# Kernel tuning notes

Measured on AMD Instinct MI355X. Metric: run time of the kernel, lower is better.

The kernel has to match this reference:

```python
import jax, jax.numpy as jnp
import numpy as np

N_NODES = 100000
N_EDGES = 1600000
EMB = 128
EDGE_DIMS = [6, 3]
BN_EPS = 1e-5


def setup_inputs() -> dict:
    key = jax.random.key(0)
    ks = jax.random.split(key, 16)
    inp = {
        "node_feats": jax.random.normal(ks[0], (N_NODES, EMB), jnp.float32),
        "edge_feat_0": jax.random.uniform(ks[1], (N_EDGES, EDGE_DIMS[0]), jnp.float32),
        "edge_feat_1": jax.random.uniform(ks[2], (N_EDGES, EDGE_DIMS[1]), jnp.float32),
        "src": jax.random.randint(ks[3], (N_EDGES,), 0, N_NODES, jnp.int32),
        "dst": jax.random.randint(ks[4], (N_EDGES,), 0, N_NODES, jnp.int32),
    }
    # edge embedding linears (MLP num_layers==1 -> plain Linear)
    s0 = 1.0 / np.sqrt(EDGE_DIMS[0])
    s1 = 1.0 / np.sqrt(EDGE_DIMS[1])
    inp["We0"] = jax.random.uniform(ks[5], (EDGE_DIMS[0], EMB), jnp.float32, -s0, s0)
    inp["be0"] = jax.random.uniform(ks[6], (EMB,), jnp.float32, -s0, s0)
    inp["We1"] = jax.random.uniform(ks[7], (EDGE_DIMS[1], EMB), jnp.float32, -s1, s1)
    inp["be1"] = jax.random.uniform(ks[8], (EMB,), jnp.float32, -s1, s1)
    # mlp: Linear(emb, 2*emb) -> ReLU -> Linear(2*emb, emb)
    sm = 1.0 / np.sqrt(EMB)
    sh = 1.0 / np.sqrt(2 * EMB)
    inp["W1"] = jax.random.uniform(ks[9], (EMB, 2 * EMB), jnp.float32, -sm, sm)
    inp["b1"] = jax.random.uniform(ks[10], (2 * EMB,), jnp.float32, -sm, sm)
    inp["W2"] = jax.random.uniform(ks[11], (2 * EMB, EMB), jnp.float32, -sh, sh)
    inp["b2"] = jax.random.uniform(ks[12], (EMB,), jnp.float32, -sh, sh)
    # batch norm affine params
    inp["gamma"] = jnp.ones((EMB,), jnp.float32)
    inp["beta"] = jnp.zeros((EMB,), jnp.float32)
    return inp


def reference(node_feats, edge_feat_0, edge_feat_1, src, dst,
              We0, be0, We1, be1, W1, b1, W2, b2, gamma, beta):
    n_nodes = node_feats.shape[0]
    # per-family edge embeddings, summed
    edge_embs = (edge_feat_0 @ We0 + be0) + (edge_feat_1 @ We1 + be1)  # [E, D]
    # u_add_e: gather src node feats, add edge emb
    msgs = node_feats[src] + edge_embs  # [E, D]
    # scatter-sum to destination nodes
    agg = jax.ops.segment_sum(msgs, dst, num_segments=n_nodes)  # [N, D]
    # MLP: Linear -> ReLU -> Linear
    h = jax.nn.relu(agg @ W1 + b1) @ W2 + b2  # [N, D]
    # BatchNorm1d (training mode: batch statistics, biased variance)
    mean = jnp.mean(h, axis=0)
    var = jnp.var(h, axis=0)
    h = (h - mean) * jax.lax.rsqrt(var + BN_EPS) * gamma + beta
    return h
```

## Files before the change

### kernel.cpp

```cpp
#include <hip/hip_runtime.h>

#define N_NODES 100000
#define N_EDGES 1600000
#define EMB 128
#define BM 16
#define NSLAB 64
#define BN_EPS 1e-5f

#define SCAN_BLK 512
#define NB_SCAN ((N_NODES + SCAN_BLK - 1) / SCAN_BLK)
#define NPAD (NB_SCAN * SCAN_BLK)

typedef short short8 __attribute__((ext_vector_type(8)));
typedef float floatx4 __attribute__((ext_vector_type(4)));

__device__ __forceinline__ ushort f2bf(float x) {
    unsigned u = __float_as_uint(x);
    u += 0x7fffu + ((u >> 16) & 1u);
    return (ushort)(u >> 16);
}
__device__ __forceinline__ float lo2f(unsigned p) {
    return __uint_as_float(p << 16);
}
__device__ __forceinline__ float hi2f(unsigned p) {
    return __uint_as_float(p & 0xffff0000u);
}

#define DPP_ADD(x, ctrl, mask) \
    ((x) + __int_as_float(__builtin_amdgcn_update_dpp(0, __float_as_int(x), ctrl, mask, 0xf, true)))

__device__ __forceinline__ float wave_sum63(float x) {
    x = DPP_ADD(x, 0x111, 0xf);
    x = DPP_ADD(x, 0x112, 0xf);
    x = DPP_ADD(x, 0x114, 0xf);
    x = DPP_ADD(x, 0x118, 0xf);
    x = DPP_ADD(x, 0x142, 0xa);
    x = DPP_ADD(x, 0x143, 0xc);
    return __int_as_float(__builtin_amdgcn_readlane(__float_as_int(x), 63));
}

__global__ __launch_bounds__(256) void setup_kernel(
    const float* __restrict__ nf, ushort* __restrict__ nfbf,
    const int* __restrict__ dst, int* __restrict__ counts,
    const float* __restrict__ W1, const float* __restrict__ W2,
    ushort* __restrict__ w1f, ushort* __restrict__ w2f)
{
    int gtid = blockIdx.x * 256 + threadIdx.x;
    long gstride = (long)gridDim.x * 256;

    if (gtid < 65536) {
        int idx = gtid;
        int i = idx & 7;
        int lane = (idx >> 3) & 63;
        int kloc = ((lane >> 4) << 3) + i;
        int nloc = lane & 15;
        if (idx < 32768) {
            int ks = (idx >> 9) & 3, nt = idx >> 11;
            w1f[idx] = f2bf(W1[(ks * 32 + kloc) * 256 + nt * 16 + nloc]);
        } else {
            int j = idx - 32768;
            int ks = (j >> 9) & 7, nt = j >> 12;
            w2f[j] = f2bf(W2[(ks * 32 + kloc) * 128 + nt * 16 + nloc]);
        }
    }

    long total = (long)N_NODES * EMB / 4;
    for (long p = gtid; p < total; p += gstride) {
        float4 v = ((const float4*)nf)[p];
        ushort4 o;
        o.x = f2bf(v.x); o.y = f2bf(v.y); o.z = f2bf(v.z); o.w = f2bf(v.w);
        ((ushort4*)nfbf)[p] = o;
    }

    for (long e = gtid; e < N_EDGES; e += gstride)
        atomicAdd(&counts[dst[e]], 1);
}

__global__ __launch_bounds__(SCAN_BLK) void scan_blocksum_kernel(
    const int* __restrict__ counts, int* __restrict__ blockSums)
{
    __shared__ int red[SCAN_BLK];
    int t = threadIdx.x;
    int i = blockIdx.x * SCAN_BLK + t;
    red[t] = (i < N_NODES) ? counts[i] : 0;
    __syncthreads();
    for (int s = SCAN_BLK / 2; s > 0; s >>= 1) {
        if (t < s) red[t] += red[t + s];
        __syncthreads();
    }
    if (t == 0) blockSums[blockIdx.x] = red[0];
}

__global__ __launch_bounds__(SCAN_BLK) void scan_final_kernel(
    const int* __restrict__ counts, const int* __restrict__ blockSums,
    int* __restrict__ offsets, int* __restrict__ cursor)
{
    __shared__ int s[SCAN_BLK];
    __shared__ int bs[256];
    int t = threadIdx.x;
    if (t < 256) bs[t] = (t < NB_SCAN) ? blockSums[t] : 0;
    __syncthreads();
    for (int off = 1; off < 256; off <<= 1) {
        int v = (t < 256 && t >= off) ? bs[t - off] : 0;
        __syncthreads();
        if (t < 256) bs[t] += v;
        __syncthreads();
    }
    int blockBase = (blockIdx.x == 0) ? 0 : bs[blockIdx.x - 1];

    int i = blockIdx.x * SCAN_BLK + t;
    int orig = (i < N_NODES) ? counts[i] : 0;
    s[t] = orig;
    __syncthreads();
    for (int off = 1; off < SCAN_BLK; off <<= 1) {
        int v = (t >= off) ? s[t - off] : 0;
        __syncthreads();
        s[t] += v;
        __syncthreads();
    }
    int excl = s[t] - orig + blockBase;
    if (i < N_NODES) { offsets[i] = excl; cursor[i] = excl; }
    if (i == N_NODES) offsets[N_NODES] = N_EDGES;
}

__global__ __launch_bounds__(256) void scatter24_kernel(
    const int* __restrict__ src, const int* __restrict__ dst,
    const float* __restrict__ ef0, const float* __restrict__ ef1,
    int* __restrict__ cursor, int* __restrict__ rec24)
{
    int e = blockIdx.x * 256 + threadIdx.x;
    if (e >= N_EDGES) return;
    int t = dst[e];
    int pos = atomicAdd(&cursor[t], 1);

    const float2* p0 = (const float2*)(ef0 + (long)e * 6);
    float2 q0 = p0[0], q1 = p0[1], q2 = p0[2];
    const float* p1 = ef1 + (long)e * 3;
    float g0 = p1[0], g1 = p1[1], g2 = p1[2];

    unsigned u0 = (unsigned)f2bf(q0.x) | ((unsigned)f2bf(q0.y) << 16);
    unsigned u1 = (unsigned)f2bf(q1.x) | ((unsigned)f2bf(q1.y) << 16);
    unsigned u2 = (unsigned)f2bf(q2.x) | ((unsigned)f2bf(q2.y) << 16);
    unsigned u3 = (unsigned)f2bf(g0)   | ((unsigned)f2bf(g1) << 16);
    unsigned u4 = (unsigned)f2bf(g2);

    int2* out = (int2*)(rec24 + (long)pos * 6);
    out[0] = make_int2(src[e], (int)u0);
    out[1] = make_int2((int)u1, (int)u2);
    out[2] = make_int2((int)u3, (int)u4);
}

__device__ __forceinline__ void gather_full_chunks(
    int& base, int end, int lane, int q, int lp,
    const int* __restrict__ rec24, const int4* __restrict__ nf16,
    float4& accA, float4& accB, float* fs)
{
    for (; base + 64 <= end; base += 64) {
        const int2* rp = (const int2*)(rec24 + (long)(base + lane) * 6);
        int2 ra = rp[0], rb = rp[1], rc = rp[2];
        int sid = ra.x;
        fs[0] += lo2f((unsigned)ra.y); fs[1] += hi2f((unsigned)ra.y);
        fs[2] += lo2f((unsigned)rb.x); fs[3] += hi2f((unsigned)rb.x);
        fs[4] += lo2f((unsigned)rb.y); fs[5] += hi2f((unsigned)rb.y);
        fs[6] += lo2f((unsigned)rc.x); fs[7] += hi2f((unsigned)rc.x);
        fs[8] += lo2f((unsigned)rc.y);
#pragma unroll 4
        for (int j = 0; j < 16; ++j) {
            int s = __shfl(sid, 4 * j + q);
            int4 nv = nf16[(long)s * 16 + lp];
            accA.x += lo2f((unsigned)nv.x); accA.y += hi2f((unsigned)nv.x);
            accA.z += lo2f((unsigned)nv.y); accA.w += hi2f((unsigned)nv.y);
            accB.x += lo2f((unsigned)nv.z); accB.y += hi2f((unsigned)nv.z);
            accB.z += lo2f((unsigned)nv.w); accB.w += hi2f((unsigned)nv.w);
        }
    }
}

__global__ __launch_bounds__(256, 8) void gather4_kernel(
    const ushort* __restrict__ nfbf, const int* __restrict__ rec24,
    const int* __restrict__ offsets,
    const float* __restrict__ We0, const float* __restrict__ be0,
    const float* __restrict__ We1, const float* __restrict__ be1,
    float* __restrict__ agg)
{
    int wv = threadIdx.x >> 6, lane = threadIdx.x & 63;
    int n0 = blockIdx.x * 8 + wv * 2;
    int q = lane >> 4, lp = lane & 15;
    const int4* nf16 = (const int4*)nfbf;

    int beg0 = offsets[n0];
    int mid  = offsets[n0 + 1];
    int end1 = offsets[n0 + 2];

    float4 a0A = make_float4(0.f, 0.f, 0.f, 0.f), a0B = a0A;
    float4 a1A = a0A, a1B = a0A;
    float fs0[9] = {}, fs1[9] = {};

    int b0 = beg0, b1 = mid;
    gather_full_chunks(b0, mid, lane, q, lp, rec24, nf16, a0A, a0B, fs0);
    gather_full_chunks(b1, end1, lane, q, lp, rec24, nf16, a1A, a1B, fs1);

    int m0 = mid - b0, m1 = end1 - b1;
    int sid0 = 0, sid1 = 0;
    if (lane < m0) {
        const int2* rp = (const int2*)(rec24 + (long)(b0 + lane) * 6);
        int2 ra = rp[0], rb = rp[1], rc = rp[2];
        sid0 = ra.x;
        fs0[0] += lo2f((unsigned)ra.y); fs0[1] += hi2f((unsigned)ra.y);
        fs0[2] += lo2f((unsigned)rb.x); fs0[3] += hi2f((unsigned)rb.x);
        fs0[4] += lo2f((unsigned)rb.y); fs0[5] += hi2f((unsigned)rb.y);
        fs0[6] += lo2f((unsigned)rc.x); fs0[7] += hi2f((unsigned)rc.x);
        fs0[8] += lo2f((unsigned)rc.y);
    }
    if (lane < m1) {
        const int2* rp = (const int2*)(rec24 + (long)(b1 + lane) * 6);
        int2 ra = rp[0], rb = rp[1], rc = rp[2];
        sid1 = ra.x;
        fs1[0] += lo2f((unsigned)ra.y); fs1[1] += hi2f((unsigned)ra.y);
        fs1[2] += lo2f((unsigned)rb.x); fs1[3] += hi2f((unsigned)rb.x);
        fs1[4] += lo2f((unsigned)rb.y); fs1[5] += hi2f((unsigned)rb.y);
        fs1[6] += lo2f((unsigned)rc.x); fs1[7] += hi2f((unsigned)rc.x);
        fs1[8] += lo2f((unsigned)rc.y);
    }
    int mx = m0 > m1 ? m0 : m1;
    int rounds = (mx + 3) >> 2;
#pragma unroll 4
    for (int j = 0; j < rounds; ++j) {
        int r = 4 * j + q;
        int s0 = __shfl(sid0, r);
        int s1 = __shfl(sid1, r);
        if (r < m0) {
            int4 nv = nf16[(long)s0 * 16 + lp];
            a0A.x += lo2f((unsigned)nv.x); a0A.y += hi2f((unsigned)nv.x);
            a0A.z += lo2f((unsigned)nv.y); a0A.w += hi2f((unsigned)nv.y);
            a0B.x += lo2f((unsigned)nv.z); a0B.y += hi2f((unsigned)nv.z);
            a0B.z += lo2f((unsigned)nv.w); a0B.w += hi2f((unsigned)nv.w);
        }
        if (r < m1) {
            int4 nv = nf16[(long)s1 * 16 + lp];
            a1A.x += lo2f((unsigned)nv.x); a1A.y += hi2f((unsigned)nv.x);
            a1A.z += lo2f((unsigned)nv.y); a1A.w += hi2f((unsigned)nv.y);
            a1B.x += lo2f((unsigned)nv.z); a1B.y += hi2f((unsigned)nv.z);
            a1B.z += lo2f((unsigned)nv.w); a1B.w += hi2f((unsigned)nv.w);
        }
    }

#define QRED(v) v += __shfl_xor(v, 16); v += __shfl_xor(v, 32);
    QRED(a0A.x) QRED(a0A.y) QRED(a0A.z) QRED(a0A.w)
    QRED(a0B.x) QRED(a0B.y) QRED(a0B.z) QRED(a0B.w)
    QRED(a1A.x) QRED(a1A.y) QRED(a1A.z) QRED(a1A.w)
    QRED(a1B.x) QRED(a1B.y) QRED(a1B.z) QRED(a1B.w)
#undef QRED

    float fk0[9], fk1[9];
#pragma unroll
    for (int k = 0; k < 9; ++k) {
        fk0[k] = wave_sum63(fs0[k]);
        fk1[k] = wave_sum63(fs1[k]);
    }

    if (q < 2) {
        bool f0 = (q == 0);
        long myn = f0 ? (long)n0 : (long)(n0 + 1);
        float deg = f0 ? (float)(mid - beg0) : (float)(end1 - mid);
        float4 accA, accB;
        accA.x = f0 ? a0A.x : a1A.x; accA.y = f0 ? a0A.y : a1A.y;
        accA.z = f0 ? a0A.z : a1A.z; accA.w = f0 ? a0A.w : a1A.w;
        accB.x = f0 ? a0B.x : a1B.x; accB.y = f0 ? a0B.y : a1B.y;
        accB.z = f0 ? a0B.z : a1B.z; accB.w = f0 ? a0B.w : a1B.w;
        float fkk[9];
#pragma unroll
        for (int k = 0; k < 9; ++k) fkk[k] = f0 ? fk0[k] : fk1[k];

        float4 bA = ((const float4*)be0)[2 * lp];
        float4 bB = ((const float4*)be0)[2 * lp + 1];
        float4 cA = ((const float4*)be1)[2 * lp];
        float4 cB = ((const float4*)be1)[2 * lp + 1];
        float4 eA, eB;
        eA.x = deg * (bA.x + cA.x); eA.y = deg * (bA.y + cA.y);
        eA.z = deg * (bA.z + cA.z); eA.w = deg * (bA.w + cA.w);
        eB.x = deg * (bB.x + cB.x); eB.y = deg * (bB.y + cB.y);
        eB.z = deg * (bB.z + cB.z); eB.w = deg * (bB.w + cB.w);
#pragma unroll
        for (int k = 0; k < 6; ++k) {
            float4 wA = ((const float4*)We0)[k * 32 + 2 * lp];
            float4 wB = ((const float4*)We0)[k * 32 + 2 * lp + 1];
            eA.x = fmaf(fkk[k], wA.x, eA.x); eA.y = fmaf(fkk[k], wA.y, eA.y);
            eA.z = fmaf(fkk[k], wA.z, eA.z); eA.w = fmaf(fkk[k], wA.w, eA.w);
            eB.x = fmaf(fkk[k], wB.x, eB.x); eB.y = fmaf(fkk[k], wB.y, eB.y);
            eB.z = fmaf(fkk[k], wB.z, eB.z); eB.w = fmaf(fkk[k], wB.w, eB.w);
        }
#pragma unroll
        for (int k = 0; k < 3; ++k) {
            float4 wA = ((const float4*)We1)[k * 32 + 2 * lp];
            float4 wB = ((const float4*)We1)[k * 32 + 2 * lp + 1];
            eA.x = fmaf(fkk[6 + k], wA.x, eA.x); eA.y = fmaf(fkk[6 + k], wA.y, eA.y);
            eA.z = fmaf(fkk[6 + k], wA.z, eA.z); eA.w = fmaf(fkk[6 + k], wA.w, eA.w);
            eB.x = fmaf(fkk[6 + k], wB.x, eB.x); eB.y = fmaf(fkk[6 + k], wB.y, eB.y);
            eB.z = fmaf(fkk[6 + k], wB.z, eB.z); eB.w = fmaf(fkk[6 + k], wB.w, eB.w);
        }
        float4 oA = make_float4(accA.x + eA.x, accA.y + eA.y, accA.z + eA.z, accA.w + eA.w);
        float4 oB = make_float4(accB.x + eB.x, accB.y + eB.y, accB.z + eB.z, accB.w + eB.w);
        ((float4*)agg)[myn * 32 + 2 * lp] = oA;
        ((float4*)agg)[myn * 32 + 2 * lp + 1] = oB;
    }
}

__global__ __launch_bounds__(256) void edge_scatter_kernel(
    const float* __restrict__ node_feats,
    const float* __restrict__ ef0,
    const float* __restrict__ ef1,
    const int* __restrict__ src,
    const int* __restrict__ dst,
    const float* __restrict__ We0, const float* __restrict__ be0,
    const float* __restrict__ We1, const float* __restrict__ be1,
    float* __restrict__ agg)
{
    __shared__ float wS[10 * EMB];
    int tid = threadIdx.x;
    for (int i = tid; i < 6 * EMB; i += 256) wS[i] = We0[i];
    for (int i = tid; i < 3 * EMB; i += 256) wS[6 * EMB + i] = We1[i];
    if (tid < EMB) wS[9 * EMB + tid] = be0[tid] + be1[tid];
    __syncthreads();

    int e = blockIdx.x * 2 + (tid >> 7);
    if (e >= N_EDGES) return;
    int d = tid & 127;
    int s = src[e];
    int t = dst[e];
    const float* f0 = ef0 + (long)e * 6;
    const float* f1 = ef1 + (long)e * 3;

    float emb = wS[9 * EMB + d];
#pragma unroll
    for (int k = 0; k < 6; ++k) emb = fmaf(f0[k], wS[k * EMB + d], emb);
#pragma unroll
    for (int k = 0; k < 3; ++k) emb = fmaf(f1[k], wS[6 * EMB + k * EMB + d], emb);

    float val = node_feats[(long)s * EMB + d] + emb;
    atomicAdd(&agg[(long)t * EMB + d], val);
}

__global__ __launch_bounds__(256) void mlp_mfma_kernel(
    float* __restrict__ h,
    const ushort* __restrict__ w1f, const ushort* __restrict__ w2f,
    const float* __restrict__ b1, const float* __restrict__ b2,
    float* __restrict__ stats)
{
    __shared__ __align__(16) char h1S[32 * 512];

    int tid = threadIdx.x;
    int lane = tid & 63;
    int wv = tid >> 6;
    long base = (long)blockIdx.x * 32;

    float4 araw[2][4][2];
#pragma unroll
    for (int mt = 0; mt < 2; ++mt)
#pragma unroll
        for (int ks = 0; ks < 4; ++ks) {
            long row = base + mt * 16 + (lane & 15);
            const float4* p = (const float4*)(h + row * EMB + ks * 32 + ((lane >> 4) << 3));
            araw[mt][ks][0] = p[0];
            araw[mt][ks][1] = p[1];
        }
    __syncthreads();

    short8 a[2][4];
#pragma unroll
    for (int mt = 0; mt < 2; ++mt)
#pragma unroll
        for (int ks = 0; ks < 4; ++ks) {
            union { ushort u[8]; short8 v; } pk;
            float4 x = araw[mt][ks][0], y = araw[mt][ks][1];
            pk.u[0] = f2bf(x.x); pk.u[1] = f2bf(x.y); pk.u[2] = f2bf(x.z); pk.u[3] = f2bf(x.w);
            pk.u[4] = f2bf(y.x); pk.u[5] = f2bf(y.y); pk.u[6] = f2bf(y.z); pk.u[7] = f2bf(y.w);
            a[mt][ks] = pk.v;
        }

    floatx4 acc1[2][4];
#pragma unroll
    for (int nt = 0; nt < 4; ++nt) {
        float bias = b1[(wv * 4 + nt) * 16 + (lane & 15)];
#pragma unroll
        for (int mt = 0; mt < 2; ++mt)
            acc1[mt][nt] = (floatx4){bias, bias, bias, bias};
    }
#pragma unroll
    for (int ks = 0; ks < 4; ++ks) {
#pragma unroll
        for (int nt = 0; nt < 4; ++nt) {
            short8 b = *(const short8*)&w1f[(((wv * 4 + nt) * 4 + ks) * 64 + lane) * 8];
            acc1[0][nt] = __builtin_amdgcn_mfma_f32_16x16x32_bf16(a[0][ks], b, acc1[0][nt], 0, 0, 0);
            acc1[1][nt] = __builtin_amdgcn_mfma_f32_16x16x32_bf16(a[1][ks], b, acc1[1][nt], 0, 0, 0);
        }
    }
#pragma unroll
    for (int mt = 0; mt < 2; ++mt)
#pragma unroll
        for (int nt = 0; nt < 4; ++nt)
#pragma unroll
            for (int i = 0; i < 4; ++i) {
                int row = mt * 16 + ((lane >> 4) << 2) + i;
                int col = (wv * 4 + nt) * 16 + (lane & 15);
                float v = fmaxf(acc1[mt][nt][i], 0.f);
                *(ushort*)&h1S[row * 512 + ((2 * col) ^ ((row & 7) << 4))] = f2bf(v);
            }
    __syncthreads();

    int swz = (lane & 7) << 4;
    floatx4 acc2[2][2];
#pragma unroll
    for (int nt = 0; nt < 2; ++nt) {
        float bias = b2[(wv * 2 + nt) * 16 + (lane & 15)];
#pragma unroll
        for (int mt = 0; mt < 2; ++mt)
            acc2[mt][nt] = (floatx4){bias, bias, bias, bias};
    }
#pragma unroll
    for (int ks = 0; ks < 8; ++ks) {
        int kb = ks * 64 + ((lane >> 4) << 4);
        short8 a0 = *(const short8*)&h1S[(lane & 15) * 512 + (kb ^ swz)];
        short8 a1 = *(const short8*)&h1S[(16 + (lane & 15)) * 512 + (kb ^ swz)];
#pragma unroll
        for (int nt = 0; nt < 2; ++nt) {
            short8 b = *(const short8*)&w2f[(((wv * 2 + nt) * 8 + ks) * 64 + lane) * 8];
            acc2[0][nt] = __builtin_amdgcn_mfma_f32_16x16x32_bf16(a0, b, acc2[0][nt], 0, 0, 0);
            acc2[1][nt] = __builtin_amdgcn_mfma_f32_16x16x32_bf16(a1, b, acc2[1][nt], 0, 0, 0);
        }
    }

    float s[2] = {0.f, 0.f}, s2[2] = {0.f, 0.f};
#pragma unroll
    for (int nt = 0; nt < 2; ++nt) {
        int col = (wv * 2 + nt) * 16 + (lane & 15);
#pragma unroll
        for (int mt = 0; mt < 2; ++mt)
#pragma unroll
            for (int i = 0; i < 4; ++i) {
                int row = mt * 16 + ((lane >> 4) << 2) + i;
                float v = acc2[mt][nt][i];
                h[(base + row) * EMB + col] = v;
                s[nt] += v;
                s2[nt] = fmaf(v, v, s2[nt]);
            }
    }
#pragma unroll
    for (int nt = 0; nt < 2; ++nt) {
        s[nt] += __shfl_xor(s[nt], 16);
        s[nt] += __shfl_xor(s[nt], 32);
        s2[nt] += __shfl_xor(s2[nt], 16);
        s2[nt] += __shfl_xor(s2[nt], 32);
    }
    if (lane < 16) {
        float* slab = stats + (blockIdx.x & (NSLAB - 1)) * (2 * EMB);
#pragma unroll
        for (int nt = 0; nt < 2; ++nt) {
            int col = (wv * 2 + nt) * 16 + lane;
            atomicAdd(&slab[col], s[nt]);
            atomicAdd(&slab[EMB + col], s2[nt]);
        }
    }
}

__global__ __launch_bounds__(256) void mlp_kernel(
    float* __restrict__ h,
    const float* __restrict__ W1, const float* __restrict__ b1,
    const float* __restrict__ W2, const float* __restrict__ b2,
    float* __restrict__ stats)
{
    __shared__ float aggS[BM][EMB];
    __shared__ float h1S[BM][2 * EMB];
    __shared__ float sredS[256];
    __shared__ float s2redS[256];

    int tid = threadIdx.x;
    long base = (long)blockIdx.x * BM;

    for (int i = tid; i < BM * EMB; i += 256)
        aggS[i >> 7][i & 127] = h[base * EMB + i];
    __syncthreads();

    {
        float acc[BM];
        float bias = b1[tid];
#pragma unroll
        for (int r = 0; r < BM; ++r) acc[r] = bias;
        for (int k = 0; k < EMB; ++k) {
            float w = W1[k * (2 * EMB) + tid];
#pragma unroll
            for (int r = 0; r < BM; ++r) acc[r] = fmaf(aggS[r][k], w, acc[r]);
        }
#pragma unroll
        for (int r = 0; r < BM; ++r) h1S[r][tid] = fmaxf(acc[r], 0.0f);
    }
    __syncthreads();

    {
        int c = tid & 127;
        int half = tid >> 7;
        float acc[8];
        float bias = b2[c];
#pragma unroll
        for (int r = 0; r < 8; ++r) acc[r] = bias;
        for (int k = 0; k < 2 * EMB; ++k) {
            float w = W2[k * EMB + c];
#pragma unroll
            for (int r = 0; r < 8; ++r) acc[r] = fmaf(h1S[half * 8 + r][k], w, acc[r]);
        }
        float s = 0.f, s2 = 0.f;
#pragma unroll
        for (int r = 0; r < 8; ++r) {
            h[(base + half * 8 + r) * EMB + c] = acc[r];
            s += acc[r];
            s2 = fmaf(acc[r], acc[r], s2);
        }
        sredS[tid] = s;
        s2redS[tid] = s2;
    }
    __syncthreads();
    if (tid < 128) {
        float s = sredS[tid] + sredS[tid + 128];
        float s2 = s2redS[tid] + s2redS[tid + 128];
        float* slab = stats + (blockIdx.x & (NSLAB - 1)) * (2 * EMB);
        atomicAdd(&slab[tid], s);
        atomicAdd(&slab[EMB + tid], s2);
    }
}

__global__ __launch_bounds__(256) void bn_apply_fused_kernel(
    float* __restrict__ h, const float* __restrict__ stats,
    const float* __restrict__ gamma, const float* __restrict__ beta)
{
    __shared__ float scS[EMB], shS[EMB];
    int tid = threadIdx.x;
    if (tid < EMB) {
        float s = 0.f, s2 = 0.f;
        for (int b = 0; b < NSLAB; ++b) {
            s += stats[b * (2 * EMB) + tid];
            s2 += stats[b * (2 * EMB) + EMB + tid];
        }
        float mean = s / (float)N_NODES;
        float var = s2 / (float)N_NODES - mean * mean;
        float sc = gamma[tid] * rsqrtf(var + BN_EPS);
        scS[tid] = sc;
        shS[tid] = beta[tid] - mean * sc;
    }
    __syncthreads();
    long total = (long)N_NODES * EMB / 4;
    long stride = (long)gridDim.x * blockDim.x;
    for (long i = (long)blockIdx.x * blockDim.x + threadIdx.x; i < total; i += stride) {
        float4 v = ((float4*)h)[i];
        int c = (int)((i * 4) & 127);
        v.x = fmaf(v.x, scS[c + 0], shS[c + 0]);
        v.y = fmaf(v.y, scS[c + 1], shS[c + 1]);
        v.z = fmaf(v.z, scS[c + 2], shS[c + 2]);
        v.w = fmaf(v.w, scS[c + 3], shS[c + 3]);
        ((float4*)h)[i] = v;
    }
}

extern "C" void kernel_launch(void* const* d_in, const int* in_sizes, int n_in,
                              void* d_out, int out_size, void* d_ws, size_t ws_size,
                              hipStream_t stream) {
    const float* node_feats = (const float*)d_in[0];
    const float* ef0 = (const float*)d_in[1];
    const float* ef1 = (const float*)d_in[2];
    const int* src = (const int*)d_in[3];
    const int* dst = (const int*)d_in[4];
    const float* We0 = (const float*)d_in[5];
    const float* be0 = (const float*)d_in[6];
    const float* We1 = (const float*)d_in[7];
    const float* be1 = (const float*)d_in[8];
    const float* W1 = (const float*)d_in[9];
    const float* b1 = (const float*)d_in[10];
    const float* W2 = (const float*)d_in[11];
    const float* b2 = (const float*)d_in[12];
    const float* gamma = (const float*)d_in[13];
    const float* beta = (const float*)d_in[14];

    float* out = (float*)d_out;

    float* stats = (float*)d_ws;
    float* scaleshift = stats + NSLAB * 2 * EMB;
    int* counts = (int*)(scaleshift + 256);
    int* offsets = counts + NPAD;
    int* cursor = offsets + NPAD;
    int* blockSums = cursor + NPAD;
    ushort* w1f = (ushort*)(blockSums + 256);
    ushort* w2f = w1f + 32768;
    int* rec24 = (int*)(w2f + 32768);
    ushort* nfbf = (ushort*)(rec24 + (size_t)N_EDGES * 6);
    size_t needed = (size_t)((char*)(nfbf + (size_t)N_NODES * EMB) - (char*)d_ws);

    if (ws_size >= needed) {
        hipMemsetAsync(d_ws, 0,
            (size_t)(NSLAB * 2 * EMB + 256) * sizeof(float) + (size_t)NPAD * sizeof(int),
            stream);
        setup_kernel<<<2048, 256, 0, stream>>>(
            node_feats, nfbf, dst, counts, W1, W2, w1f, w2f);
        scan_blocksum_kernel<<<NB_SCAN, SCAN_BLK, 0, stream>>>(counts, blockSums);
        scan_final_kernel<<<NB_SCAN, SCAN_BLK, 0, stream>>>(counts, blockSums, offsets, cursor);
        scatter24_kernel<<<(N_EDGES + 255) / 256, 256, 0, stream>>>(
            src, dst, ef0, ef1, cursor, rec24);
        gather4_kernel<<<N_NODES / 8, 256, 0, stream>>>(
            nfbf, rec24, offsets, We0, be0, We1, be1, out);
        mlp_mfma_kernel<<<N_NODES / 32, 256, 0, stream>>>(
            out, w1f, w2f, b1, b2, stats);
    } else {
        hipMemsetAsync(stats, 0, (size_t)NSLAB * 2 * EMB * sizeof(float), stream);
        hipMemsetAsync(d_out, 0, (size_t)N_NODES * EMB * sizeof(float), stream);
        edge_scatter_kernel<<<N_EDGES / 2, 256, 0, stream>>>(
            node_feats, ef0, ef1, src, dst, We0, be0, We1, be1, out);
        mlp_kernel<<<N_NODES / BM, 256, 0, stream>>>(out, W1, b1, W2, b2, stats);
    }

    bn_apply_fused_kernel<<<4096, 256, 0, stream>>>(out, stats, gamma, beta);
}
```

Before: 349.6 us.

## Store MLP output as bf16 scratch and apply BN from bf16 buffer

The MLP kernel now writes its pre-BatchNorm output as bf16 into the reused edge-record workspace instead of fp32 into the output buffer. A new bn_apply kernel reads those bf16 values and writes normalized fp32 output, which cuts the intermediate read and write traffic roughly in half. The gather kernel's epilogue is also reworked so all four quarter-waves each store one float4 rather than two quarters storing two, and the MLP drops a __syncthreads. The cost is that h is rounded to bf16 before normalization, which adds error, and the scratch buffer aliases rec24.

```diff
diff --git a/kernel.cpp b/kernel.cpp
--- a/kernel.cpp
+++ b/kernel.cpp
@@ -259,51 +259,42 @@
         fk1[k] = wave_sum63(fs1[k]);
     }
 
-    if (q < 2) {
-        bool f0 = (q == 0);
-        long myn = f0 ? (long)n0 : (long)(n0 + 1);
-        float deg = f0 ? (float)(mid - beg0) : (float)(end1 - mid);
-        float4 accA, accB;
-        accA.x = f0 ? a0A.x : a1A.x; accA.y = f0 ? a0A.y : a1A.y;
-        accA.z = f0 ? a0A.z : a1A.z; accA.w = f0 ? a0A.w : a1A.w;
-        accB.x = f0 ? a0B.x : a1B.x; accB.y = f0 ? a0B.y : a1B.y;
-        accB.z = f0 ? a0B.z : a1B.z; accB.w = f0 ? a0B.w : a1B.w;
-        float fkk[9];
-#pragma unroll
-        for (int k = 0; k < 9; ++k) fkk[k] = f0 ? fk0[k] : fk1[k];
-
-        float4 bA = ((const float4*)be0)[2 * lp];
-        float4 bB = ((const float4*)be0)[2 * lp + 1];
-        float4 cA = ((const float4*)be1)[2 * lp];
-        float4 cB = ((const float4*)be1)[2 * lp + 1];
-        float4 eA, eB;
-        eA.x = deg * (bA.x + cA.x); eA.y = deg * (bA.y + cA.y);
-        eA.z = deg * (bA.z + cA.z); eA.w = deg * (bA.w + cA.w);
-        eB.x = deg * (bB.x + cB.x); eB.y = deg * (bB.y + cB.y);
-        eB.z = deg * (bB.z + cB.z); eB.w = deg * (bB.w + cB.w);
-#pragma unroll
-        for (int k = 0; k < 6; ++k) {
-            float4 wA = ((const float4*)We0)[k * 32 + 2 * lp];
-            float4 wB = ((const float4*)We0)[k * 32 + 2 * lp + 1];
-            eA.x = fmaf(fkk[k], wA.x, eA.x); eA.y = fmaf(fkk[k], wA.y, eA.y);
-            eA.z = fmaf(fkk[k], wA.z, eA.z); eA.w = fmaf(fkk[k], wA.w, eA.w);
-            eB.x = fmaf(fkk[k], wB.x, eB.x); eB.y = fmaf(fkk[k], wB.y, eB.y);
-            eB.z = fmaf(fkk[k], wB.z, eB.z); eB.w = fmaf(fkk[k], wB.w, eB.w);
-        }
-#pragma unroll
-        for (int k = 0; k < 3; ++k) {
-            float4 wA = ((const float4*)We1)[k * 32 + 2 * lp];
-            float4 wB = ((const float4*)We1)[k * 32 + 2 * lp + 1];
-            eA.x = fmaf(fkk[6 + k], wA.x, eA.x); eA.y = fmaf(fkk[6 + k], wA.y, eA.y);
-            eA.z = fmaf(fkk[6 + k], wA.z, eA.z); eA.w = fmaf(fkk[6 + k], wA.w, eA.w);
-            eB.x = fmaf(fkk[6 + k], wB.x, eB.x); eB.y = fmaf(fkk[6 + k], wB.y, eB.y);
-            eB.z = fmaf(fkk[6 + k], wB.z, eB.z); eB.w = fmaf(fkk[6 + k], wB.w, eB.w);
-        }
-        float4 oA = make_float4(accA.x + eA.x, accA.y + eA.y, accA.z + eA.z, accA.w + eA.w);
-        float4 oB = make_float4(accB.x + eB.x, accB.y + eB.y, accB.z + eB.z, accB.w + eB.w);
-        ((float4*)agg)[myn * 32 + 2 * lp] = oA;
-        ((float4*)agg)[myn * 32 + 2 * lp + 1] = oB;
-    }
+    int nodesel = q & 1;
+    int hh = q >> 1;
+    long myn = (long)n0 + nodesel;
+    float deg = nodesel ? (float)(end1 - mid) : (float)(mid - beg0);
+    float4 acc;
+    {
+        float4 selA, selB;
+        selA.x = nodesel ? a1A.x : a0A.x; selA.y = nodesel ? a1A.y : a0A.y;
+        selA.z = nodesel ? a1A.z : a0A.z; selA.w = nodesel ? a1A.w : a0A.w;
+        selB.x = nodesel ? a1B.x : a0B.x; selB.y = nodesel ? a1B.y : a0B.y;
+        selB.z = nodesel ? a1B.z : a0B.z; selB.w = nodesel ? a1B.w : a0B.w;
+        acc.x = hh ? selB.x : selA.x; acc.y = hh ? selB.y : selA.y;
+        acc.z = hh ? selB.z : selA.z; acc.w = hh ? selB.w : selA.w;
+    }
+    int fidx = 2 * lp + hh;
+    float4 bb0 = ((const float4*)be0)[fidx];
+    float4 bb1 = ((const float4*)be1)[fidx];
+    float4 e;
+    e.x = deg * (bb0.x + bb1.x); e.y = deg * (bb0.y + bb1.y);
+    e.z = deg * (bb0.z + bb1.z); e.w = deg * (bb0.w + bb1.w);
+#pragma unroll
+    for (int k = 0; k < 6; ++k) {
+        float f = nodesel ? fk1[k] : fk0[k];
+        float4 w = ((const float4*)We0)[k * 32 + fidx];
+        e.x = fmaf(f, w.x, e.x); e.y = fmaf(f, w.y, e.y);
+        e.z = fmaf(f, w.z, e.z); e.w = fmaf(f, w.w, e.w);
+    }
+#pragma unroll
+    for (int k = 0; k < 3; ++k) {
+        float f = nodesel ? fk1[6 + k] : fk0[6 + k];
+        float4 w = ((const float4*)We1)[k * 32 + fidx];
+        e.x = fmaf(f, w.x, e.x); e.y = fmaf(f, w.y, e.y);
+        e.z = fmaf(f, w.z, e.z); e.w = fmaf(f, w.w, e.w);
+    }
+    float4 o = make_float4(acc.x + e.x, acc.y + e.y, acc.z + e.z, acc.w + e.w);
+    ((float4*)agg)[myn * 32 + fidx] = o;
 }
 
 __global__ __launch_bounds__(256) void edge_scatter_kernel(
@@ -342,7 +333,7 @@
 }
 
 __global__ __launch_bounds__(256) void mlp_mfma_kernel(
-    float* __restrict__ h,
+    const float* __restrict__ aggf, ushort* __restrict__ hbf,
     const ushort* __restrict__ w1f, const ushort* __restrict__ w2f,
     const float* __restrict__ b1, const float* __restrict__ b2,
     float* __restrict__ stats)
@@ -354,25 +345,15 @@
     int wv = tid >> 6;
     long base = (long)blockIdx.x * 32;
 
-    float4 araw[2][4][2];
+    short8 a[2][4];
 #pragma unroll
     for (int mt = 0; mt < 2; ++mt)
 #pragma unroll
         for (int ks = 0; ks < 4; ++ks) {
             long row = base + mt * 16 + (lane & 15);
-            const float4* p = (const float4*)(h + row * EMB + ks * 32 + ((lane >> 4) << 3));
-            araw[mt][ks][0] = p[0];
-            araw[mt][ks][1] = p[1];
-        }
-    __syncthreads();
-
-    short8 a[2][4];
-#pragma unroll
-    for (int mt = 0; mt < 2; ++mt)
-#pragma unroll
-        for (int ks = 0; ks < 4; ++ks) {
+            const float4* p = (const float4*)(aggf + row * EMB + ks * 32 + ((lane >> 4) << 3));
+            float4 x = p[0], y = p[1];
             union { ushort u[8]; short8 v; } pk;
-            float4 x = araw[mt][ks][0], y = araw[mt][ks][1];
             pk.u[0] = f2bf(x.x); pk.u[1] = f2bf(x.y); pk.u[2] = f2bf(x.z); pk.u[3] = f2bf(x.w);
             pk.u[4] = f2bf(y.x); pk.u[5] = f2bf(y.y); pk.u[6] = f2bf(y.z); pk.u[7] = f2bf(y.w);
             a[mt][ks] = pk.v;
@@ -440,7 +421,7 @@
             for (int i = 0; i < 4; ++i) {
                 int row = mt * 16 + ((lane >> 4) << 2) + i;
                 float v = acc2[mt][nt][i];
-                h[(base + row) * EMB + col] = v;
+                hbf[(base + row) * EMB + col] = f2bf(v);
                 s[nt] += v;
                 s2[nt] = fmaf(v, v, s2[nt]);
             }
@@ -525,6 +506,45 @@
         float* slab = stats + (blockIdx.x & (NSLAB - 1)) * (2 * EMB);
         atomicAdd(&slab[tid], s);
         atomicAdd(&slab[EMB + tid], s2);
+    }
+}
+
+__global__ __launch_bounds__(256) void bn_apply_bf16_kernel(
+    const ushort* __restrict__ hbf, float* __restrict__ out,
+    const float* __restrict__ stats,
+    const float* __restrict__ gamma, const float* __restrict__ beta)
+{
+    __shared__ float scS[EMB], shS[EMB];
+    int tid = threadIdx.x;
+    if (tid < EMB) {
+        float s = 0.f, s2 = 0.f;
+        for (int b = 0; b < NSLAB; ++b) {
+            s += stats[b * (2 * EMB) + tid];
+            s2 += stats[b * (2 * EMB) + EMB + tid];
+        }
+        float mean = s / (float)N_NODES;
+        float var = s2 / (float)N_NODES - mean * mean;
+        float sc = gamma[tid] * rsqrtf(var + BN_EPS);
+        scS[tid] = sc;
+        shS[tid] = beta[tid] - mean * sc;
+    }
+    __syncthreads();
+    long total = (long)N_NODES * EMB / 8;
+    long stride = (long)gridDim.x * blockDim.x;
+    for (long p = (long)blockIdx.x * blockDim.x + threadIdx.x; p < total; p += stride) {
+        uint4 v = ((const uint4*)hbf)[p];
+        int c = (int)((p * 8) & 127);
+        float4 o1, o2;
+        o1.x = fmaf(lo2f(v.x), scS[c + 0], shS[c + 0]);
+        o1.y = fmaf(hi2f(v.x), scS[c + 1], shS[c + 1]);
+        o1.z = fmaf(lo2f(v.y), scS[c + 2], shS[c + 2]);
+        o1.w = fmaf(hi2f(v.y), scS[c + 3], shS[c + 3]);
+        o2.x = fmaf(lo2f(v.z), scS[c + 4], shS[c + 4]);
+        o2.y = fmaf(hi2f(v.z), scS[c + 5], shS[c + 5]);
+        o2.z = fmaf(lo2f(v.w), scS[c + 6], shS[c + 6]);
+        o2.w = fmaf(hi2f(v.w), scS[c + 7], shS[c + 7]);
+        ((float4*)out)[2 * p] = o1;
+        ((float4*)out)[2 * p + 1] = o2;
     }
 }
 
@@ -590,6 +610,7 @@
     ushort* w1f = (ushort*)(blockSums + 256);
     ushort* w2f = w1f + 32768;
     int* rec24 = (int*)(w2f + 32768);
+    ushort* hbf = (ushort*)rec24;
     ushort* nfbf = (ushort*)(rec24 + (size_t)N_EDGES * 6);
     size_t needed = (size_t)((char*)(nfbf + (size_t)N_NODES * EMB) - (char*)d_ws);
 
@@ -606,14 +627,14 @@
         gather4_kernel<<<N_NODES / 8, 256, 0, stream>>>(
             nfbf, rec24, offsets, We0, be0, We1, be1, out);
         mlp_mfma_kernel<<<N_NODES / 32, 256, 0, stream>>>(
-            out, w1f, w2f, b1, b2, stats);
+            out, hbf, w1f, w2f, b1, b2, stats);
+        bn_apply_bf16_kernel<<<1024, 256, 0, stream>>>(hbf, out, stats, gamma, beta);
     } else {
         hipMemsetAsync(stats, 0, (size_t)NSLAB * 2 * EMB * sizeof(float), stream);
         hipMemsetAsync(d_out, 0, (size_t)N_NODES * EMB * sizeof(float), stream);
         edge_scatter_kernel<<<N_EDGES / 2, 256, 0, stream>>>(
             node_feats, ef0, ef1, src, dst, We0, be0, We1, be1, out);
         mlp_kernel<<<N_NODES / BM, 256, 0, stream>>>(out, W1, b1, W2, b2, stats);
-    }
-
-    bn_apply_fused_kernel<<<4096, 256, 0, stream>>>(out, stats, gamma, beta);
-}
+        bn_apply_fused_kernel<<<4096, 256, 0, stream>>>(out, stats, gamma, beta);
+    }
+}
```

After: 317.4 us. 1.1x faster.
